# Performance work log

Measured on AMD Instinct MI355X. Metric: run time of the kernel, lower is better.

The kernel has to match this reference:

```python
import jax, jax.numpy as jnp
import numpy as np

D_MODEL = 768
HEADS = 12
D_K = D_MODEL // HEADS
NEG = -1e9


def setup_inputs() -> dict:
    key = jax.random.key(0)
    ks = jax.random.split(key, 7)
    B, S, D = 4, 2048, D_MODEL
    scale = 1.0 / np.sqrt(D)
    q = jax.random.normal(ks[0], (B, S, D), dtype=jnp.float32)
    k = jax.random.normal(ks[1], (B, S, D), dtype=jnp.float32)
    v = jax.random.normal(ks[2], (B, S, D), dtype=jnp.float32)
    # causal mask, broadcastable over batch and heads; mask==0 -> -1e9
    mask = jnp.tril(jnp.ones((1, 1, S, S), dtype=jnp.int32))
    W_q = jax.random.normal(ks[3], (D, D), dtype=jnp.float32) * scale
    W_k = jax.random.normal(ks[4], (D, D), dtype=jnp.float32) * scale
    W_v = jax.random.normal(ks[5], (D, D), dtype=jnp.float32) * scale
    W_o = jax.random.normal(ks[6], (D, D), dtype=jnp.float32) * scale
    return {"q": q, "k": k, "v": v, "mask": mask,
            "W_q": W_q, "W_k": W_k, "W_v": W_v, "W_o": W_o}


def reference(q, k, v, mask, W_q, W_k, W_v, W_o):
    B, S, D = q.shape
    # nn.Linear(bias=False): y = x @ W.T
    query = (q @ W_q.T).reshape(B, S, HEADS, D_K).transpose(0, 2, 1, 3)  # [B,H,S,dk]
    key_ = (k @ W_k.T).reshape(B, S, HEADS, D_K).transpose(0, 2, 1, 3)
    value = (v @ W_v.T).reshape(B, S, HEADS, D_K).transpose(0, 2, 1, 3)
    scores = jnp.einsum('bhqd,bhkd->bhqk', query, key_) / jnp.sqrt(
        jnp.asarray(D_K, dtype=query.dtype))
    scores = jnp.where(mask == 0, jnp.asarray(NEG, dtype=scores.dtype), scores)
    attn = jax.nn.softmax(scores, axis=-1)
    # dropout rate = 0.0 (inference / eval mode): identity
    x = jnp.einsum('bhqk,bhkd->bhqd', attn, value)  # [B,H,S,dk]
    x = x.transpose(0, 2, 1, 3).reshape(B, S, D)
    return x @ W_o.T
```

## Files before the change

### kernel.cpp

```cpp
#include <hip/hip_runtime.h>


typedef _Float16 f16x8 __attribute__((ext_vector_type(8)));
typedef _Float16 f16x4 __attribute__((ext_vector_type(4)));
typedef float floatx4 __attribute__((ext_vector_type(4)));

#define MFMA16(a, b, c) __builtin_amdgcn_mfma_f32_16x16x32_f16((a), (b), (c), 0, 0, 0)

static constexpr int B_ = 4;
static constexpr int S_ = 2048;
static constexpr int D_ = 768;
static constexpr int H_ = 12;
static constexpr int DK = 64;

__device__ __forceinline__ f16x8 cvt8(float4 a, float4 b) {
  f16x8 h;
  h[0] = (_Float16)a.x; h[1] = (_Float16)a.y;
  h[2] = (_Float16)a.z; h[3] = (_Float16)a.w;
  h[4] = (_Float16)b.x; h[5] = (_Float16)b.y;
  h[6] = (_Float16)b.z; h[7] = (_Float16)b.w;
  return h;
}

__device__ __forceinline__ void dma16(const _Float16* g, _Float16* l) {
  __builtin_amdgcn_global_load_lds(
      (const __attribute__((address_space(1))) unsigned int*)g,
      (__attribute__((address_space(3))) unsigned int*)l, 16, 0, 0);
}

struct CvtArgs {
  const float* src[7];
  _Float16* dst[7];
  int end[7];
  int nseg;
};

__global__ __launch_bounds__(256) void cvt_f32_f16(CvtArgs a) {
  int b = blockIdx.x;
  int s = 0;
  while (s < a.nseg - 1 && b >= a.end[s]) ++s;
  int local = b - (s ? a.end[s - 1] : 0);
  const int tid = threadIdx.x;
  const float4* p = (const float4*)(a.src[s] + (size_t)local * 2048) + tid * 2;
  float4 x0 = p[0], x1 = p[1];
  *(f16x8*)(a.dst[s] + (size_t)local * 2048 + tid * 8) = cvt8(x0, x1);
}

static constexpr int PAN = 128 * 32;

struct QkvPtrs {
  const void* a[3];
  const void* w[3];
};

template <int MODE, bool SCALE>
__device__ __forceinline__ void gemm_core64(const _Float16* __restrict__ A,
                                            const _Float16* __restrict__ Bm,
                                            void* __restrict__ Cv,
                                            _Float16* As, _Float16* Bs,
                                            int m0, int n0, int N, int K) {
  const int tid = threadIdx.x;
  const int wave = tid >> 6, lane = tid & 63;
  const int l15 = lane & 15, quad = lane >> 4;
  const int wm = (wave >> 1) * 64, wn = (wave & 1) * 64;
  const int lr = lane >> 2;
  const int lc = (lane & 3) * 8;

  floatx4 acc[4][4] = {};

  const int wb = wave * 16;

  for (int k0 = 0; k0 < K; k0 += 64) {
    {
      const _Float16* g = A + (size_t)(m0 + wb + lr) * K + k0 + lc;
      dma16(g, As + wb * 32);
      dma16(g + 32, As + PAN + wb * 32);
      const _Float16* g2 = g + (size_t)64 * K;
      dma16(g2, As + (64 + wb) * 32);
      dma16(g2 + 32, As + PAN + (64 + wb) * 32);
    }
    {
      const _Float16* g = Bm + (size_t)(n0 + wb + lr) * K + k0 + lc;
      dma16(g, Bs + wb * 32);
      dma16(g + 32, Bs + PAN + wb * 32);
      const _Float16* g2 = g + (size_t)64 * K;
      dma16(g2, Bs + (64 + wb) * 32);
      dma16(g2 + 32, Bs + PAN + (64 + wb) * 32);
    }
    __syncthreads();

#pragma unroll
    for (int p = 0; p < 2; ++p) {
      f16x8 af[4], bf[4];
#pragma unroll
      for (int t = 0; t < 4; ++t)
        af[t] = *(const f16x8*)(As + p * PAN + (wm + t * 16 + l15) * 32 +
                                quad * 8);
#pragma unroll
      for (int t = 0; t < 4; ++t)
        bf[t] = *(const f16x8*)(Bs + p * PAN + (wn + t * 16 + l15) * 32 +
                                quad * 8);
#pragma unroll
      for (int mt = 0; mt < 4; ++mt)
#pragma unroll
        for (int nt = 0; nt < 4; ++nt)
          acc[mt][nt] = MFMA16(af[mt], bf[nt], acc[mt][nt]);
    }
    __syncthreads();
  }

  if constexpr (MODE == 2) {
#pragma unroll
    for (int mt = 0; mt < 4; ++mt)
#pragma unroll
      for (int nt = 0; nt < 4; ++nt) {
        int row = m0 + wm + mt * 16 + quad * 4;
        int col = n0 + wn + nt * 16 + l15;
        int b = row >> 11, s = row & 2047;
        int h = col >> 6, d = col & 63;
        f16x4 v4;
#pragma unroll
        for (int r = 0; r < 4; ++r) v4[r] = (_Float16)acc[mt][nt][r];
        *(f16x4*)((_Float16*)Cv + ((size_t)(b * H_ + h) * DK + d) * S_ + s) =
            v4;
      }
  } else {
#pragma unroll
    for (int mt = 0; mt < 4; ++mt)
#pragma unroll
      for (int nt = 0; nt < 4; ++nt)
#pragma unroll
        for (int r = 0; r < 4; ++r) {
          int row = m0 + wm + mt * 16 + quad * 4 + r;
          int col = n0 + wn + nt * 16 + l15;
          float val = acc[mt][nt][r];
          if constexpr (SCALE) val *= 0.125f;
          if constexpr (MODE == 0) {
            ((float*)Cv)[(size_t)row * N + col] = val;
          } else {
            int b = row >> 11, s = row & 2047;
            int h = col >> 6, d = col & 63;
            ((_Float16*)Cv)[((size_t)(b * H_ + h) * S_ + s) * DK + d] =
                (_Float16)val;
          }
        }
  }
}

__global__ __launch_bounds__(256) void qkv_gemm64(QkvPtrs P, _Float16* Qh,
                                                  _Float16* Kh, _Float16* Vt) {
  __shared__ _Float16 As[2 * PAN];
  __shared__ _Float16 Bs[2 * PAN];
  const int z = blockIdx.z;
  const int m0 = blockIdx.y * 128, n0 = blockIdx.x * 128;
  if (z == 0) {
    gemm_core64<1, true>((const _Float16*)P.a[0], (const _Float16*)P.w[0], Qh,
                         As, Bs, m0, n0, D_, D_);
  } else if (z == 1) {
    gemm_core64<1, false>((const _Float16*)P.a[1], (const _Float16*)P.w[1], Kh,
                          As, Bs, m0, n0, D_, D_);
  } else {
    gemm_core64<2, false>((const _Float16*)P.a[2], (const _Float16*)P.w[2], Vt,
                          As, Bs, m0, n0, D_, D_);
  }
}

__global__ __launch_bounds__(256) void gemm_out64(const _Float16* A,
                                                  const _Float16* W,
                                                  float* C) {
  __shared__ _Float16 As[2 * PAN];
  __shared__ _Float16 Bs[2 * PAN];
  gemm_core64<0, false>(A, W, C, As, Bs, blockIdx.y * 128, blockIdx.x * 128,
                        D_, D_);
}

template <int AP, int BP, int MODE, bool SCALE>
__global__ __launch_bounds__(256) void gemm128(const void* __restrict__ Av,
                                               const void* __restrict__ Bv,
                                               void* __restrict__ Cv,
                                               int M, int N, int K) {
  constexpr int SA = AP ? 32 : 40;
  constexpr int SB = BP ? 32 : 40;
  __shared__ _Float16 As[128 * 40];
  __shared__ _Float16 Bs[128 * 40];

  const int tid = threadIdx.x;
  const int wave = tid >> 6, lane = tid & 63;
  const int l15 = lane & 15, quad = lane >> 4;
  const int wm = (wave >> 1) * 64, wn = (wave & 1) * 64;
  const int m0 = blockIdx.y * 128, n0 = blockIdx.x * 128;

  const int srow = tid >> 1, scol = (tid & 1) * 16;
  const int c0 = wave * 64 + lane, c1 = 256 + wave * 64 + lane;
  const int r0 = c0 >> 2, cc0 = (c0 & 3) * 8;
  const int r1 = c1 >> 2, cc1 = (c1 & 3) * 8;

  floatx4 acc[4][4] = {};

  for (int k0 = 0; k0 < K; k0 += 32) {
    if constexpr (AP == 1) {
      const _Float16* A = (const _Float16*)Av;
      dma16(A + (size_t)(m0 + r0) * K + k0 + cc0, As + wave * 64 * 8);
      dma16(A + (size_t)(m0 + r1) * K + k0 + cc1, As + (256 + wave * 64) * 8);
    } else {
      const float* A = (const float*)Av;
      const float4* p = (const float4*)(A + (size_t)(m0 + srow) * K + k0 + scol);
      float4 x0 = p[0], x1 = p[1], x2 = p[2], x3 = p[3];
      *(f16x8*)(As + srow * 40 + scol) = cvt8(x0, x1);
      *(f16x8*)(As + srow * 40 + scol + 8) = cvt8(x2, x3);
    }
    if constexpr (BP == 1) {
      const _Float16* Bp = (const _Float16*)Bv;
      dma16(Bp + (size_t)(n0 + r0) * K + k0 + cc0, Bs + wave * 64 * 8);
      dma16(Bp + (size_t)(n0 + r1) * K + k0 + cc1, Bs + (256 + wave * 64) * 8);
    } else {
      const float* Bp = (const float*)Bv;
      const float4* p =
          (const float4*)(Bp + (size_t)(n0 + srow) * K + k0 + scol);
      float4 x0 = p[0], x1 = p[1], x2 = p[2], x3 = p[3];
      *(f16x8*)(Bs + srow * 40 + scol) = cvt8(x0, x1);
      *(f16x8*)(Bs + srow * 40 + scol + 8) = cvt8(x2, x3);
    }
    __syncthreads();

    f16x8 af[4], bf[4];
#pragma unroll
    for (int t = 0; t < 4; ++t)
      af[t] = *(const f16x8*)(As + (wm + t * 16 + l15) * SA + quad * 8);
#pragma unroll
    for (int t = 0; t < 4; ++t)
      bf[t] = *(const f16x8*)(Bs + (wn + t * 16 + l15) * SB + quad * 8);
#pragma unroll
    for (int mt = 0; mt < 4; ++mt)
#pragma unroll
      for (int nt = 0; nt < 4; ++nt)
        acc[mt][nt] = MFMA16(af[mt], bf[nt], acc[mt][nt]);
    __syncthreads();
  }

#pragma unroll
  for (int mt = 0; mt < 4; ++mt)
#pragma unroll
    for (int nt = 0; nt < 4; ++nt)
#pragma unroll
      for (int r = 0; r < 4; ++r) {
        int row = m0 + wm + mt * 16 + quad * 4 + r;
        int col = n0 + wn + nt * 16 + l15;
        float val = acc[mt][nt][r];
        if constexpr (SCALE) val *= 0.125f;
        if constexpr (MODE == 0) {
          ((float*)Cv)[(size_t)row * N + col] = val;
        } else if constexpr (MODE == 1) {
          int b = row >> 11, s = row & 2047;
          int h = col >> 6, d = col & 63;
          ((_Float16*)Cv)[((size_t)(b * H_ + h) * S_ + s) * DK + d] =
              (_Float16)val;
        } else {
          int b = col >> 11, s = col & 2047;
          int h = row >> 6, d = row & 63;
          ((_Float16*)Cv)[((size_t)(b * H_ + h) * DK + d) * S_ + s] =
              (_Float16)val;
        }
      }
}

template <int AP, int BP>
__global__ __launch_bounds__(256) void qkv_gemm(QkvPtrs P, _Float16* Qh,
                                                _Float16* Kh, _Float16* Vt) {
  constexpr int SA = AP ? 32 : 40;
  constexpr int SB = BP ? 32 : 40;
  constexpr int K = 768;
  __shared__ _Float16 As[128 * 40];
  __shared__ _Float16 Bs[128 * 40];

  const int z = blockIdx.z;
  const void* Av = P.a[z];
  const void* Bv = P.w[z];

  const int tid = threadIdx.x;
  const int wave = tid >> 6, lane = tid & 63;
  const int l15 = lane & 15, quad = lane >> 4;
  const int wm = (wave >> 1) * 64, wn = (wave & 1) * 64;
  const int m0 = blockIdx.y * 128, n0 = blockIdx.x * 128;

  const int srow = tid >> 1, scol = (tid & 1) * 16;
  const int c0 = wave * 64 + lane, c1 = 256 + wave * 64 + lane;
  const int r0 = c0 >> 2, cc0 = (c0 & 3) * 8;
  const int r1 = c1 >> 2, cc1 = (c1 & 3) * 8;

  floatx4 acc[4][4] = {};

  for (int k0 = 0; k0 < K; k0 += 32) {
    if constexpr (AP == 1) {
      const _Float16* A = (const _Float16*)Av;
      dma16(A + (size_t)(m0 + r0) * K + k0 + cc0, As + wave * 64 * 8);
      dma16(A + (size_t)(m0 + r1) * K + k0 + cc1, As + (256 + wave * 64) * 8);
    } else {
      const float* A = (const float*)Av;
      const float4* p = (const float4*)(A + (size_t)(m0 + srow) * K + k0 + scol);
      float4 x0 = p[0], x1 = p[1], x2 = p[2], x3 = p[3];
      *(f16x8*)(As + srow * 40 + scol) = cvt8(x0, x1);
      *(f16x8*)(As + srow * 40 + scol + 8) = cvt8(x2, x3);
    }
    if constexpr (BP == 1) {
      const _Float16* Bp = (const _Float16*)Bv;
      dma16(Bp + (size_t)(n0 + r0) * K + k0 + cc0, Bs + wave * 64 * 8);
      dma16(Bp + (size_t)(n0 + r1) * K + k0 + cc1, Bs + (256 + wave * 64) * 8);
    } else {
      const float* Bp = (const float*)Bv;
      const float4* p =
          (const float4*)(Bp + (size_t)(n0 + srow) * K + k0 + scol);
      float4 x0 = p[0], x1 = p[1], x2 = p[2], x3 = p[3];
      *(f16x8*)(Bs + srow * 40 + scol) = cvt8(x0, x1);
      *(f16x8*)(Bs + srow * 40 + scol + 8) = cvt8(x2, x3);
    }
    __syncthreads();

    f16x8 af[4], bf[4];
#pragma unroll
    for (int t = 0; t < 4; ++t)
      af[t] = *(const f16x8*)(As + (wm + t * 16 + l15) * SA + quad * 8);
#pragma unroll
    for (int t = 0; t < 4; ++t)
      bf[t] = *(const f16x8*)(Bs + (wn + t * 16 + l15) * SB + quad * 8);
#pragma unroll
    for (int mt = 0; mt < 4; ++mt)
#pragma unroll
      for (int nt = 0; nt < 4; ++nt)
        acc[mt][nt] = MFMA16(af[mt], bf[nt], acc[mt][nt]);
    __syncthreads();
  }

  const float scale = (z == 0) ? 0.125f : 1.0f;
  if (z < 2) {
    _Float16* C = z ? Kh : Qh;
#pragma unroll
    for (int mt = 0; mt < 4; ++mt)
#pragma unroll
      for (int nt = 0; nt < 4; ++nt)
#pragma unroll
        for (int r = 0; r < 4; ++r) {
          int row = m0 + wm + mt * 16 + quad * 4 + r;
          int col = n0 + wn + nt * 16 + l15;
          int b = row >> 11, s = row & 2047;
          int h = col >> 6, d = col & 63;
          C[((size_t)(b * H_ + h) * S_ + s) * DK + d] =
              (_Float16)(acc[mt][nt][r] * scale);
        }
  } else {
#pragma unroll
    for (int mt = 0; mt < 4; ++mt)
#pragma unroll
      for (int nt = 0; nt < 4; ++nt) {
        int row = m0 + wm + mt * 16 + quad * 4;
        int col = n0 + wn + nt * 16 + l15;
        int b = row >> 11, s = row & 2047;
        int h = col >> 6, d = col & 63;
        f16x4 v4;
#pragma unroll
        for (int r = 0; r < 4; ++r) v4[r] = (_Float16)acc[mt][nt][r];
        *(f16x4*)(Vt + ((size_t)(b * H_ + h) * DK + d) * S_ + s) = v4;
      }
  }
}

__global__ __launch_bounds__(256, 4) void flash_attn(
    const _Float16* __restrict__ Qh, const _Float16* __restrict__ Kh,
    const _Float16* __restrict__ Vt, _Float16* __restrict__ Oh) {
  __shared__ _Float16 Ks[64 * 72];
  __shared__ _Float16 Vts[64 * 72];
  __shared__ _Float16 Ps[4][16 * 36];

  const int tid = threadIdx.x;
  const int wave = tid >> 6, lane = tid & 63;
  const int l15 = lane & 15, quad = lane >> 4;

  const int linear = blockIdx.x + gridDim.x * blockIdx.y;
  const int xcd = linear & 7;
  const int seq = linear >> 3;
  const int bh = xcd * 6 + (seq >> 4);
  const int xp = seq & 15;
  const int b = bh / H_, h = bh % H_;
  const size_t base = (size_t)bh * S_ * DK;
  const size_t basev = (size_t)bh * DK * S_;

  const int srow = tid >> 2;
  const int sc0 = (tid & 3) * 16;

  for (int c = 0; c < 2; ++c) {
    const int qt = c ? xp : 31 - xp;
    const int q0 = qt * 64;
    const int qrow = q0 + wave * 16 + l15;
    f16x8 qf0 = *(const f16x8*)(Qh + base + (size_t)qrow * DK + quad * 8);
    f16x8 qf1 = *(const f16x8*)(Qh + base + (size_t)qrow * DK + 32 + quad * 8);

    floatx4 o_acc[4] = {};
    float plsum[4] = {0.f, 0.f, 0.f, 0.f};

    const _Float16* ks = Kh + base + (size_t)srow * DK + sc0;
    const _Float16* vs = Vt + basev + (size_t)srow * S_ + sc0;
    f16x8 pk0 = *(const f16x8*)ks;
    f16x8 pk1 = *(const f16x8*)(ks + 8);
    f16x8 pv0 = *(const f16x8*)vs;
    f16x8 pv1 = *(const f16x8*)(vs + 8);

    for (int j = 0; j <= qt; ++j) {
      __syncthreads();
      *(f16x8*)(Ks + srow * 72 + sc0) = pk0;
      *(f16x8*)(Ks + srow * 72 + sc0 + 8) = pk1;
      *(f16x8*)(Vts + srow * 72 + sc0) = pv0;
      *(f16x8*)(Vts + srow * 72 + sc0 + 8) = pv1;
      __syncthreads();

      if (j < qt) {
        const _Float16* kn =
            Kh + base + (size_t)((j + 1) * 64 + srow) * DK + sc0;
        const _Float16* vn =
            Vt + basev + (size_t)srow * S_ + (j + 1) * 64 + sc0;
        pk0 = *(const f16x8*)kn;
        pk1 = *(const f16x8*)(kn + 8);
        pv0 = *(const f16x8*)vn;
        pv1 = *(const f16x8*)(vn + 8);
      }

      floatx4 s_acc[4] = {};
#pragma unroll
      for (int t = 0; t < 4; ++t) {
        f16x8 kf0 = *(const f16x8*)(Ks + (t * 16 + l15) * 72 + quad * 8);
        f16x8 kf1 = *(const f16x8*)(Ks + (t * 16 + l15) * 72 + 32 + quad * 8);
        s_acc[t] = MFMA16(qf0, kf0, s_acc[t]);
        s_acc[t] = MFMA16(qf1, kf1, s_acc[t]);
      }

      const bool diag = (j == qt);
      const int j0 = j * 64;
      float p[4][4];
#pragma unroll
      for (int t = 0; t < 4; ++t)
#pragma unroll
        for (int r = 0; r < 4; ++r) {
          float s = s_acc[t][r];
          if (diag) {
            int rg = q0 + wave * 16 + quad * 4 + r;
            int cg = j0 + t * 16 + l15;
            if (cg > rg) s = -1e30f;
          }
          float e = __expf(s);
          p[t][r] = e;
          plsum[r] += e;
        }

#pragma unroll
      for (int t = 0; t < 2; ++t)
#pragma unroll
        for (int r = 0; r < 4; ++r)
          Ps[wave][(quad * 4 + r) * 36 + t * 16 + l15] = (_Float16)p[t][r];
      f16x8 pf0 = *(const f16x8*)(Ps[wave] + l15 * 36 + quad * 8);
#pragma unroll
      for (int t = 0; t < 4; ++t) {
        f16x8 vf0 = *(const f16x8*)(Vts + (t * 16 + l15) * 72 + quad * 8);
        o_acc[t] = MFMA16(pf0, vf0, o_acc[t]);
      }
#pragma unroll
      for (int t = 2; t < 4; ++t)
#pragma unroll
        for (int r = 0; r < 4; ++r)
          Ps[wave][(quad * 4 + r) * 36 + (t - 2) * 16 + l15] =
              (_Float16)p[t][r];
      f16x8 pf1 = *(const f16x8*)(Ps[wave] + l15 * 36 + quad * 8);
#pragma unroll
      for (int t = 0; t < 4; ++t) {
        f16x8 vf1 = *(const f16x8*)(Vts + (t * 16 + l15) * 72 + 32 + quad * 8);
        o_acc[t] = MFMA16(pf1, vf1, o_acc[t]);
      }
    }

#pragma unroll
    for (int r = 0; r < 4; ++r) {
      float l = plsum[r];
      l += __shfl_xor(l, 1);
      l += __shfl_xor(l, 2);
      l += __shfl_xor(l, 4);
      l += __shfl_xor(l, 8);
      float inv = 1.0f / l;
      int row = q0 + wave * 16 + quad * 4 + r;
#pragma unroll
      for (int t = 0; t < 4; ++t) {
        float val = o_acc[t][r] * inv;
        Oh[((size_t)(b * S_ + row)) * D_ + h * DK + t * 16 + l15] =
            (_Float16)val;
      }
    }
  }
}

extern "C" void kernel_launch(void* const* d_in, const int* in_sizes, int n_in,
                              void* d_out, int out_size, void* d_ws,
                              size_t ws_size, hipStream_t stream) {
  const float* q = (const float*)d_in[0];
  const float* k = (const float*)d_in[1];
  const float* v = (const float*)d_in[2];
  const float* Wq = (const float*)d_in[4];
  const float* Wk = (const float*)d_in[5];
  const float* Wv = (const float*)d_in[6];
  const float* Wo = (const float*)d_in[7];
  float* out = (float*)d_out;

  const size_t E = (size_t)B_ * H_ * S_ * DK;
  const size_t EW = (size_t)D_ * D_;
  _Float16* Qh = (_Float16*)d_ws;
  _Float16* Kh = Qh + E;
  _Float16* Vt = Kh + E;
  _Float16* Oh = Vt + E;

  const int M = B_ * S_;
  dim3 blk(256);
  dim3 qg(D_ / 128, M / 128, 3);
  dim3 pg(D_ / 128, M / 128);
  dim3 fg(16, B_ * H_);

  const size_t need_full = (7 * E + 4 * EW) * 2;
  const size_t need_w = (4 * E + 4 * EW) * 2;

  if (ws_size >= need_full) {
    _Float16* qf = Oh + E;
    _Float16* kf = qf + E;
    _Float16* vf = kf + E;
    _Float16* wqf = vf + E;
    _Float16* wkf = wqf + EW;
    _Float16* wvf = wkf + EW;
    _Float16* wof = wvf + EW;
    CvtArgs ca;
    ca.src[0] = q;  ca.dst[0] = qf;
    ca.src[1] = k;  ca.dst[1] = kf;
    ca.src[2] = v;  ca.dst[2] = vf;
    ca.src[3] = Wq; ca.dst[3] = wqf;
    ca.src[4] = Wk; ca.dst[4] = wkf;
    ca.src[5] = Wv; ca.dst[5] = wvf;
    ca.src[6] = Wo; ca.dst[6] = wof;
    int ends[7] = {3072, 6144, 9216, 9504, 9792, 10080, 10368};
    for (int i = 0; i < 7; ++i) ca.end[i] = ends[i];
    ca.nseg = 7;
    cvt_f32_f16<<<10368, blk, 0, stream>>>(ca);
    QkvPtrs P;
    P.a[0] = qf; P.a[1] = kf; P.a[2] = vf;
    P.w[0] = wqf; P.w[1] = wkf; P.w[2] = wvf;
    qkv_gemm64<<<qg, blk, 0, stream>>>(P, Qh, Kh, Vt);
    flash_attn<<<fg, blk, 0, stream>>>(Qh, Kh, Vt, Oh);
    gemm_out64<<<pg, blk, 0, stream>>>(Oh, wof, out);
  } else if (ws_size >= need_w) {
    _Float16* wqf = Oh + E;
    _Float16* wkf = wqf + EW;
    _Float16* wvf = wkf + EW;
    _Float16* wof = wvf + EW;
    CvtArgs ca;
    ca.src[0] = Wq; ca.dst[0] = wqf;
    ca.src[1] = Wk; ca.dst[1] = wkf;
    ca.src[2] = Wv; ca.dst[2] = wvf;
    ca.src[3] = Wo; ca.dst[3] = wof;
    int ends[4] = {288, 576, 864, 1152};
    for (int i = 0; i < 4; ++i) ca.end[i] = ends[i];
    ca.nseg = 4;
    cvt_f32_f16<<<1152, blk, 0, stream>>>(ca);
    QkvPtrs P;
    P.a[0] = q; P.a[1] = k; P.a[2] = v;
    P.w[0] = wqf; P.w[1] = wkf; P.w[2] = wvf;
    qkv_gemm<0, 1><<<qg, blk, 0, stream>>>(P, Qh, Kh, Vt);
    flash_attn<<<fg, blk, 0, stream>>>(Qh, Kh, Vt, Oh);
    gemm128<1, 1, 0, false><<<pg, blk, 0, stream>>>(Oh, wof, out, M, D_, D_);
  } else {
    QkvPtrs P;
    P.a[0] = q; P.a[1] = k; P.a[2] = v;
    P.w[0] = Wq; P.w[1] = Wk; P.w[2] = Wv;
    qkv_gemm<0, 0><<<qg, blk, 0, stream>>>(P, Qh, Kh, Vt);
    flash_attn<<<fg, blk, 0, stream>>>(Qh, Kh, Vt, Oh);
    gemm128<1, 0, 0, false><<<pg, blk, 0, stream>>>(Oh, Wo, out, M, D_, D_);
  }
}
```

Baseline: 263.0 us.

## Halve GEMM M-tile and load flash-attention K/V fragments directly from global

The QKV and output GEMMs switch from 128x128 to 64x128 tiles, which doubles the block count for better CU occupancy and wave balance. Flash attention drops its shared-memory staging of K and V tiles along with the register prefetch. Each wave now loads its MFMA K/V fragments straight from global memory, relying on L2/L1 caching, and launch bounds drop to 3 blocks per CU. The aim is to remove LDS round-trips and block-wide syncs, at the cost of redundant global loads across the four waves and no software prefetch.

```diff
diff --git a/kernel.cpp b/kernel.cpp
--- a/kernel.cpp
+++ b/kernel.cpp
@@ -46,7 +46,8 @@
   *(f16x8*)(a.dst[s] + (size_t)local * 2048 + tid * 8) = cvt8(x0, x1);
 }
 
-static constexpr int PAN = 128 * 32;
+static constexpr int PAN_A = 64 * 32;
+static constexpr int PAN_B = 128 * 32;
 
 struct QkvPtrs {
   const void* a[3];
@@ -54,54 +55,49 @@
 };
 
 template <int MODE, bool SCALE>
-__device__ __forceinline__ void gemm_core64(const _Float16* __restrict__ A,
-                                            const _Float16* __restrict__ Bm,
-                                            void* __restrict__ Cv,
-                                            _Float16* As, _Float16* Bs,
-                                            int m0, int n0, int N, int K) {
+__device__ __forceinline__ void gemm_core(const _Float16* __restrict__ A,
+                                          const _Float16* __restrict__ Bm,
+                                          void* __restrict__ Cv, _Float16* As,
+                                          _Float16* Bs, int m0, int n0, int N,
+                                          int K) {
   const int tid = threadIdx.x;
   const int wave = tid >> 6, lane = tid & 63;
   const int l15 = lane & 15, quad = lane >> 4;
-  const int wm = (wave >> 1) * 64, wn = (wave & 1) * 64;
+  const int wm = (wave >> 1) * 32, wn = (wave & 1) * 64;
   const int lr = lane >> 2;
   const int lc = (lane & 3) * 8;
 
-  floatx4 acc[4][4] = {};
-
-  const int wb = wave * 16;
+  floatx4 acc[2][4] = {};
 
   for (int k0 = 0; k0 < K; k0 += 64) {
-    {
-      const _Float16* g = A + (size_t)(m0 + wb + lr) * K + k0 + lc;
-      dma16(g, As + wb * 32);
-      dma16(g + 32, As + PAN + wb * 32);
-      const _Float16* g2 = g + (size_t)64 * K;
-      dma16(g2, As + (64 + wb) * 32);
-      dma16(g2 + 32, As + PAN + (64 + wb) * 32);
-    }
-    {
-      const _Float16* g = Bm + (size_t)(n0 + wb + lr) * K + k0 + lc;
-      dma16(g, Bs + wb * 32);
-      dma16(g + 32, Bs + PAN + wb * 32);
-      const _Float16* g2 = g + (size_t)64 * K;
-      dma16(g2, Bs + (64 + wb) * 32);
-      dma16(g2 + 32, Bs + PAN + (64 + wb) * 32);
-    }
+#pragma unroll
+    for (int p = 0; p < 2; ++p) {
+      const _Float16* g = A + (size_t)(m0 + wave * 16 + lr) * K + k0 + p * 32 + lc;
+      dma16(g, As + p * PAN_A + wave * 16 * 32);
+    }
+#pragma unroll
+    for (int p = 0; p < 2; ++p)
+#pragma unroll
+      for (int q = 0; q < 2; ++q) {
+        const _Float16* g =
+            Bm + (size_t)(n0 + wave * 32 + q * 16 + lr) * K + k0 + p * 32 + lc;
+        dma16(g, Bs + p * PAN_B + (wave * 32 + q * 16) * 32);
+      }
     __syncthreads();
 
 #pragma unroll
     for (int p = 0; p < 2; ++p) {
-      f16x8 af[4], bf[4];
+      f16x8 af[2], bf[4];
+#pragma unroll
+      for (int t = 0; t < 2; ++t)
+        af[t] = *(const f16x8*)(As + p * PAN_A + (wm + t * 16 + l15) * 32 +
+                                quad * 8);
 #pragma unroll
       for (int t = 0; t < 4; ++t)
-        af[t] = *(const f16x8*)(As + p * PAN + (wm + t * 16 + l15) * 32 +
+        bf[t] = *(const f16x8*)(Bs + p * PAN_B + (wn + t * 16 + l15) * 32 +
                                 quad * 8);
 #pragma unroll
-      for (int t = 0; t < 4; ++t)
-        bf[t] = *(const f16x8*)(Bs + p * PAN + (wn + t * 16 + l15) * 32 +
-                                quad * 8);
-#pragma unroll
-      for (int mt = 0; mt < 4; ++mt)
+      for (int mt = 0; mt < 2; ++mt)
 #pragma unroll
         for (int nt = 0; nt < 4; ++nt)
           acc[mt][nt] = MFMA16(af[mt], bf[nt], acc[mt][nt]);
@@ -111,7 +107,7 @@
 
   if constexpr (MODE == 2) {
 #pragma unroll
-    for (int mt = 0; mt < 4; ++mt)
+    for (int mt = 0; mt < 2; ++mt)
 #pragma unroll
       for (int nt = 0; nt < 4; ++nt) {
         int row = m0 + wm + mt * 16 + quad * 4;
@@ -126,7 +122,7 @@
       }
   } else {
 #pragma unroll
-    for (int mt = 0; mt < 4; ++mt)
+    for (int mt = 0; mt < 2; ++mt)
 #pragma unroll
       for (int nt = 0; nt < 4; ++nt)
 #pragma unroll
@@ -147,38 +143,37 @@
   }
 }
 
-__global__ __launch_bounds__(256) void qkv_gemm64(QkvPtrs P, _Float16* Qh,
+__global__ __launch_bounds__(256) void gemm_qkv64(QkvPtrs P, _Float16* Qh,
                                                   _Float16* Kh, _Float16* Vt) {
-  __shared__ _Float16 As[2 * PAN];
-  __shared__ _Float16 Bs[2 * PAN];
+  __shared__ _Float16 As[2 * PAN_A];
+  __shared__ _Float16 Bs[2 * PAN_B];
   const int z = blockIdx.z;
-  const int m0 = blockIdx.y * 128, n0 = blockIdx.x * 128;
+  const int m0 = blockIdx.y * 64, n0 = blockIdx.x * 128;
   if (z == 0) {
-    gemm_core64<1, true>((const _Float16*)P.a[0], (const _Float16*)P.w[0], Qh,
-                         As, Bs, m0, n0, D_, D_);
+    gemm_core<1, true>((const _Float16*)P.a[0], (const _Float16*)P.w[0], Qh,
+                       As, Bs, m0, n0, D_, D_);
   } else if (z == 1) {
-    gemm_core64<1, false>((const _Float16*)P.a[1], (const _Float16*)P.w[1], Kh,
-                          As, Bs, m0, n0, D_, D_);
+    gemm_core<1, false>((const _Float16*)P.a[1], (const _Float16*)P.w[1], Kh,
+                        As, Bs, m0, n0, D_, D_);
   } else {
-    gemm_core64<2, false>((const _Float16*)P.a[2], (const _Float16*)P.w[2], Vt,
-                          As, Bs, m0, n0, D_, D_);
-  }
-}
-
-__global__ __launch_bounds__(256) void gemm_out64(const _Float16* A,
-                                                  const _Float16* W,
-                                                  float* C) {
-  __shared__ _Float16 As[2 * PAN];
-  __shared__ _Float16 Bs[2 * PAN];
-  gemm_core64<0, false>(A, W, C, As, Bs, blockIdx.y * 128, blockIdx.x * 128,
-                        D_, D_);
+    gemm_core<2, false>((const _Float16*)P.a[2], (const _Float16*)P.w[2], Vt,
+                        As, Bs, m0, n0, D_, D_);
+  }
+}
+
+__global__ __launch_bounds__(256) void gemm_o64(const _Float16* A,
+                                                const _Float16* W, float* C) {
+  __shared__ _Float16 As[2 * PAN_A];
+  __shared__ _Float16 Bs[2 * PAN_B];
+  gemm_core<0, false>(A, W, C, As, Bs, blockIdx.y * 64, blockIdx.x * 128, D_,
+                      D_);
 }
 
 template <int AP, int BP, int MODE, bool SCALE>
 __global__ __launch_bounds__(256) void gemm128(const void* __restrict__ Av,
                                                const void* __restrict__ Bv,
-                                               void* __restrict__ Cv,
-                                               int M, int N, int K) {
+                                               void* __restrict__ Cv, int M,
+                                               int N, int K) {
   constexpr int SA = AP ? 32 : 40;
   constexpr int SB = BP ? 32 : 40;
   __shared__ _Float16 As[128 * 40];
@@ -364,11 +359,9 @@
   }
 }
 
-__global__ __launch_bounds__(256, 4) void flash_attn(
+__global__ __launch_bounds__(256, 3) void flash_attn(
     const _Float16* __restrict__ Qh, const _Float16* __restrict__ Kh,
     const _Float16* __restrict__ Vt, _Float16* __restrict__ Oh) {
-  __shared__ _Float16 Ks[64 * 72];
-  __shared__ _Float16 Vts[64 * 72];
   __shared__ _Float16 Ps[4][16 * 36];
 
   const int tid = threadIdx.x;
@@ -384,9 +377,6 @@
   const size_t base = (size_t)bh * S_ * DK;
   const size_t basev = (size_t)bh * DK * S_;
 
-  const int srow = tid >> 2;
-  const int sc0 = (tid & 3) * 16;
-
   for (int c = 0; c < 2; ++c) {
     const int qt = c ? xp : 31 - xp;
     const int q0 = qt * 64;
@@ -397,43 +387,33 @@
     floatx4 o_acc[4] = {};
     float plsum[4] = {0.f, 0.f, 0.f, 0.f};
 
-    const _Float16* ks = Kh + base + (size_t)srow * DK + sc0;
-    const _Float16* vs = Vt + basev + (size_t)srow * S_ + sc0;
-    f16x8 pk0 = *(const f16x8*)ks;
-    f16x8 pk1 = *(const f16x8*)(ks + 8);
-    f16x8 pv0 = *(const f16x8*)vs;
-    f16x8 pv1 = *(const f16x8*)(vs + 8);
-
     for (int j = 0; j <= qt; ++j) {
-      __syncthreads();
-      *(f16x8*)(Ks + srow * 72 + sc0) = pk0;
-      *(f16x8*)(Ks + srow * 72 + sc0 + 8) = pk1;
-      *(f16x8*)(Vts + srow * 72 + sc0) = pv0;
-      *(f16x8*)(Vts + srow * 72 + sc0 + 8) = pv1;
-      __syncthreads();
-
-      if (j < qt) {
-        const _Float16* kn =
-            Kh + base + (size_t)((j + 1) * 64 + srow) * DK + sc0;
-        const _Float16* vn =
-            Vt + basev + (size_t)srow * S_ + (j + 1) * 64 + sc0;
-        pk0 = *(const f16x8*)kn;
-        pk1 = *(const f16x8*)(kn + 8);
-        pv0 = *(const f16x8*)vn;
-        pv1 = *(const f16x8*)(vn + 8);
+      __builtin_amdgcn_s_barrier();
+      const int j0 = j * 64;
+
+      f16x8 kf0[4], kf1[4];
+#pragma unroll
+      for (int t = 0; t < 4; ++t) {
+        const _Float16* kp = Kh + base + (size_t)(j0 + t * 16 + l15) * DK;
+        kf0[t] = *(const f16x8*)(kp + quad * 8);
+        kf1[t] = *(const f16x8*)(kp + 32 + quad * 8);
+      }
+      f16x8 vf0[4], vf1[4];
+#pragma unroll
+      for (int t = 0; t < 4; ++t) {
+        const _Float16* vp = Vt + basev + (size_t)(t * 16 + l15) * S_ + j0;
+        vf0[t] = *(const f16x8*)(vp + quad * 8);
+        vf1[t] = *(const f16x8*)(vp + 32 + quad * 8);
       }
 
       floatx4 s_acc[4] = {};
 #pragma unroll
       for (int t = 0; t < 4; ++t) {
-        f16x8 kf0 = *(const f16x8*)(Ks + (t * 16 + l15) * 72 + quad * 8);
-        f16x8 kf1 = *(const f16x8*)(Ks + (t * 16 + l15) * 72 + 32 + quad * 8);
-        s_acc[t] = MFMA16(qf0, kf0, s_acc[t]);
-        s_acc[t] = MFMA16(qf1, kf1, s_acc[t]);
+        s_acc[t] = MFMA16(qf0, kf0[t], s_acc[t]);
+        s_acc[t] = MFMA16(qf1, kf1[t], s_acc[t]);
       }
 
       const bool diag = (j == qt);
-      const int j0 = j * 64;
       float p[4][4];
 #pragma unroll
       for (int t = 0; t < 4; ++t)
@@ -457,10 +437,7 @@
           Ps[wave][(quad * 4 + r) * 36 + t * 16 + l15] = (_Float16)p[t][r];
       f16x8 pf0 = *(const f16x8*)(Ps[wave] + l15 * 36 + quad * 8);
 #pragma unroll
-      for (int t = 0; t < 4; ++t) {
-        f16x8 vf0 = *(const f16x8*)(Vts + (t * 16 + l15) * 72 + quad * 8);
-        o_acc[t] = MFMA16(pf0, vf0, o_acc[t]);
-      }
+      for (int t = 0; t < 4; ++t) o_acc[t] = MFMA16(pf0, vf0[t], o_acc[t]);
 #pragma unroll
       for (int t = 2; t < 4; ++t)
 #pragma unroll
@@ -469,10 +446,7 @@
               (_Float16)p[t][r];
       f16x8 pf1 = *(const f16x8*)(Ps[wave] + l15 * 36 + quad * 8);
 #pragma unroll
-      for (int t = 0; t < 4; ++t) {
-        f16x8 vf1 = *(const f16x8*)(Vts + (t * 16 + l15) * 72 + 32 + quad * 8);
-        o_acc[t] = MFMA16(pf1, vf1, o_acc[t]);
-      }
+      for (int t = 0; t < 4; ++t) o_acc[t] = MFMA16(pf1, vf1[t], o_acc[t]);
     }
 
 #pragma unroll
@@ -515,6 +489,8 @@
 
   const int M = B_ * S_;
   dim3 blk(256);
+  dim3 qg64(D_ / 128, M / 64, 3);
+  dim3 og64(D_ / 128, M / 64);
   dim3 qg(D_ / 128, M / 128, 3);
   dim3 pg(D_ / 128, M / 128);
   dim3 fg(16, B_ * H_);
@@ -545,9 +521,9 @@
     QkvPtrs P;
     P.a[0] = qf; P.a[1] = kf; P.a[2] = vf;
     P.w[0] = wqf; P.w[1] = wkf; P.w[2] = wvf;
-    qkv_gemm64<<<qg, blk, 0, stream>>>(P, Qh, Kh, Vt);
+    gemm_qkv64<<<qg64, blk, 0, stream>>>(P, Qh, Kh, Vt);
     flash_attn<<<fg, blk, 0, stream>>>(Qh, Kh, Vt, Oh);
-    gemm_out64<<<pg, blk, 0, stream>>>(Oh, wof, out);
+    gemm_o64<<<og64, blk, 0, stream>>>(Oh, wof, out);
   } else if (ws_size >= need_w) {
     _Float16* wqf = Oh + E;
     _Float16* wkf = wqf + EW;
```

Result: slower. 388.8 us (+47.8%).
